# Kernel tuning notes

Measured on AMD Instinct MI355X. Metric: run time of the kernel, lower is better.

## Reference

```python
import jax, jax.numpy as jnp
from jax import lax
import numpy as np

NUM_TAGS = 16
B, S = 512, 4096


def setup_inputs() -> dict:
    key = jax.random.key(0)
    k1, k2, k3, k4, k5 = jax.random.split(key, 5)
    emissions = jax.random.normal(k1, (B, S, NUM_TAGS), dtype=jnp.float32)
    tags = jax.random.randint(k2, (B, S), 0, NUM_TAGS, dtype=jnp.int64)
    mask = jnp.ones((B, S), dtype=bool)
    transitions = jax.random.normal(k3, (NUM_TAGS, NUM_TAGS), dtype=jnp.float32)
    start_transitions = jax.random.normal(k4, (NUM_TAGS,), dtype=jnp.float32)
    end_transitions = jax.random.normal(k5, (NUM_TAGS,), dtype=jnp.float32)
    return {
        "emissions": emissions,
        "tags": tags,
        "mask": mask,
        "transitions": transitions,
        "start_transitions": start_transitions,
        "end_transitions": end_transitions,
    }


def _forward_algorithm(emissions, mask, transitions, start_transitions, end_transitions):
    # emissions: [B,S,T], mask: [B,S] bool
    alphas0 = start_transitions[None, :] + emissions[:, 0]  # [B,T]

    def step(alphas, inp):
        emit_t, mask_t = inp  # [B,T], [B]
        # next_tag_var[b, prev, next] = alphas[b,prev] + transitions[prev,next] + emit[b,next]
        nxt = alphas[:, :, None] + transitions[None, :, :] + emit_t[:, None, :]
        new_alphas = jax.nn.logsumexp(nxt, axis=1)  # [B,T]
        alphas = jnp.where(mask_t[:, None], new_alphas, alphas)
        return alphas, None

    xs = (jnp.swapaxes(emissions, 0, 1)[1:], jnp.swapaxes(mask, 0, 1)[1:])
    alphas, _ = lax.scan(step, alphas0, xs)
    alphas = alphas + end_transitions[None, :]
    return jax.nn.logsumexp(alphas, axis=1)  # [B]


def _score_sentence(emissions, tags, mask, transitions, start_transitions, end_transitions):
    # vectorized version of the per-step torch loop (same math)
    emit_scores = jnp.take_along_axis(emissions, tags[:, :, None], axis=2)[..., 0]  # [B,S]
    trans_scores = transitions[tags[:, :-1], tags[:, 1:]]  # [B,S-1]
    maskf = mask.astype(emissions.dtype)
    scores = start_transitions[tags[:, 0]] + emit_scores[:, 0]
    scores = scores + jnp.sum((trans_scores + emit_scores[:, 1:]) * maskf[:, 1:], axis=1)
    last_valid_idx = jnp.sum(mask.astype(jnp.int32), axis=1) - 1  # [B]
    last_tag = jnp.take_along_axis(tags, last_valid_idx[:, None].astype(tags.dtype), axis=1)[:, 0]
    scores = scores + end_transitions[last_tag]
    return scores  # [B]


def reference(emissions, tags, mask, transitions, start_transitions, end_transitions):
    forward_score = _forward_algorithm(emissions, mask, transitions, start_transitions, end_transitions)
    gold_score = _score_sentence(emissions, tags, mask, transitions, start_transitions, end_transitions)
    return jnp.mean(forward_score - gold_score)  # CRF negative log-likelihood
```

## Files before the change

kernel.cpp:

```cpp
#include <hip/hip_runtime.h>

#define NT 16
#define BB 512
#define SS 4096
#define CL 128
#define NCHAIN 4
#define CLC (CL/NCHAIN)
#define NCH 32
#define NCHUNKS (BB*NCH)
#define NGRP 8
#define NGROUPS (NCHUNKS/NGRP)
#define NSUP (NCH/NGRP)
#define LOG2E 1.44269504088896340736f
#define LN2   0.69314718055994530942f

typedef float v4f __attribute__((ext_vector_type(4)));
typedef float v2f __attribute__((ext_vector_type(2)));
typedef short v4s __attribute__((ext_vector_type(4)));
typedef unsigned v2u __attribute__((ext_vector_type(2)));

#define MFMA16(A,B,C) __builtin_amdgcn_mfma_f32_16x16x16bf16_1k(A,B,C,0,0,0)

static __device__ __forceinline__ unsigned pk2bf(float x, float y) {
    return __builtin_amdgcn_perm(__float_as_uint(y), __float_as_uint(x),
                                 0x07060302u);
}

static __device__ __forceinline__ v4s identity_bfrag(int g, int j) {
    unsigned lo = 0u, hi = 0u;
    if (4 * g + 0 == j) lo |= 0x3F80u;
    if (4 * g + 1 == j) lo |= 0x3F800000u;
    if (4 * g + 2 == j) hi |= 0x3F80u;
    if (4 * g + 3 == j) hi |= 0x3F800000u;
    v2u bp; bp.x = lo; bp.y = hi;
    return __builtin_bit_cast(v4s, bp);
}

__global__ __launch_bounds__(256) void k_chunks(
    const float* __restrict__ em, const int* __restrict__ tags,
    const float* __restrict__ trans, const float* __restrict__ startt,
    const float* __restrict__ endt,
    float* __restrict__ ws_mat, float* __restrict__ ws_gold,
    float* __restrict__ ws_scale)
{
    __shared__ float wbuf[4][CL * NT];
    const int lane  = threadIdx.x & 63;
    const int wv    = threadIdx.x >> 6;
    const int chunk = blockIdx.x * 4 + wv;
    const int b = chunk >> 5;
    const int c = chunk & 31;
    const int j = lane & 15;
    const int g = lane >> 4;
    const int t0 = c * CL + 1;
    const int nst = min(CL, (SS - 1) - c * CL);

    const float* erow = em + (size_t)b * SS * NT;
    float* wf = wbuf[wv];

    {
        const float4* gp4 = (const float4*)(erow + t0 * NT);
        const int maxf = (((SS - t0) * NT) >> 2) - 1;
        #pragma unroll
        for (int kk = 0; kk < (CL * NT / 4) / 64; ++kk) {
            const int f = lane + kk * 64;
            const float4 x = gp4[min(f, maxf)];
            float4 e;
            e.x = __builtin_amdgcn_exp2f(x.x * LOG2E);
            e.y = __builtin_amdgcn_exp2f(x.y * LOG2E);
            e.z = __builtin_amdgcn_exp2f(x.z * LOG2E);
            e.w = __builtin_amdgcn_exp2f(x.w * LOG2E);
            *(float4*)(wf + (f << 2)) = e;
        }
    }

    v2u apc;
    apc.x = pk2bf(
        __builtin_amdgcn_exp2f(trans[(4*g+0)*NT + j] * LOG2E - 5.0f),
        __builtin_amdgcn_exp2f(trans[(4*g+1)*NT + j] * LOG2E - 5.0f));
    apc.y = pk2bf(
        __builtin_amdgcn_exp2f(trans[(4*g+2)*NT + j] * LOG2E - 5.0f),
        __builtin_amdgcn_exp2f(trans[(4*g+3)*NT + j] * LOG2E - 5.0f));
    const v4s afrag = __builtin_bit_cast(v4s, apc);

    v4s bf[NCHAIN];
    v4f ac[NCHAIN];
    #pragma unroll
    for (int q = 0; q < NCHAIN; ++q) {
        bf[q] = identity_bfrag(g, j);
        ac[q] = (v4f){0.f, 0.f, 0.f, 0.f};
    }
    const float* wg = wf + 4 * g;

    #define STEP(q, s) do {                                                \
        v4f t = MFMA16(afrag, bf[q], ((v4f){0.f, 0.f, 0.f, 0.f}));         \
        const float4 w4 = *(const float4*)(wg + (s) * NT);                 \
        t[0] *= w4.x; t[1] *= w4.y; t[2] *= w4.z; t[3] *= w4.w;            \
        ac[q] = t;                                                         \
        v2u p;                                                             \
        p.x = pk2bf(t[0], t[1]);                                           \
        p.y = pk2bf(t[2], t[3]);                                           \
        bf[q] = __builtin_bit_cast(v4s, p);                                \
    } while (0)

    if (nst == CL) {
        #pragma unroll 2
        for (int s = 0; s < CLC; ++s) {
            STEP(0, s);
            STEP(1, CLC + s);
            STEP(2, 2 * CLC + s);
            STEP(3, 3 * CLC + s);
        }
    } else {
        #pragma unroll
        for (int q = 0; q < NCHAIN; ++q) {
            const int lo = q * CLC, hi = min(lo + CLC, nst);
            for (int s = lo; s < hi; ++s) STEP(q, s);
        }
    }
    #undef STEP

    #pragma unroll
    for (int q = 1; q < NCHAIN; ++q)
        #pragma unroll
        for (int r = 0; r < 4; ++r)
            wf[(q - 1) * 256 + (4 * g + r) * NT + j] = ac[q][r];

    v4s run = bf[0];
    v4f accf = ac[0];
    #pragma unroll
    for (int q = 1; q < NCHAIN; ++q) {
        const float4 x = *(const float4*)(wf + (q - 1) * 256 + j * NT + 4 * g);
        v2u ap;
        ap.x = pk2bf(x.x, x.y);
        ap.y = pk2bf(x.z, x.w);
        accf = MFMA16(__builtin_bit_cast(v4s, ap), run,
                      ((v4f){0.f, 0.f, 0.f, 0.f}));
        v2u p;
        p.x = pk2bf(accf[0], accf[1]);
        p.y = pk2bf(accf[2], accf[3]);
        run = __builtin_bit_cast(v4s, p);
    }

    const unsigned u0 = __builtin_amdgcn_readfirstlane(__float_as_uint(accf[0]));
    const int kk = (int)((u0 >> 23) & 0xffu) - 127;
    const float sc = __uint_as_float((unsigned)(127 - kk) << 23);
    float* mp = ws_mat + ((size_t)chunk << 8);
    #pragma unroll
    for (int r = 0; r < 4; ++r)
        mp[(4 * g + r) * NT + j] = accf[r] * sc;
    if (lane == 0) ws_scale[chunk] = (float)kk;

    const int* tg = tags + b * SS;
    float gp = 0.f;
    {
        int t = t0 + lane;
        if (lane < nst) {
            const int tt = tg[t], tp = tg[t - 1];
            gp = trans[tp * NT + tt] + erow[t * NT + tt];
            if (t == SS - 1) gp += endt[tt];
        }
        t = t0 + 64 + lane;
        if (64 + lane < nst) {
            const int tt = tg[t], tp = tg[t - 1];
            gp += trans[tp * NT + tt] + erow[t * NT + tt];
            if (t == SS - 1) gp += endt[tt];
        }
    }
    if (c == 0 && lane == 0) {
        const int z = tg[0];
        gp += startt[z] + erow[z];
    }
    #pragma unroll
    for (int m = 32; m > 0; m >>= 1) gp += __shfl_xor(gp, m, 64);
    if (lane == 0) ws_gold[chunk] = gp;
}

__global__ __launch_bounds__(256) void k_group(
    const float* __restrict__ ws_mat, float* __restrict__ ws2)
{
    const int lane = threadIdx.x & 63;
    const int wid  = blockIdx.x * 4 + (threadIdx.x >> 6);
    const int j = lane & 15;
    const int g = lane >> 4;
    const float* src = ws_mat + ((size_t)wid << 11) + (j << 4) + (g << 2);

    v4s bfrag = identity_bfrag(g, j);
    v4f acc = {0.f, 0.f, 0.f, 0.f};

    #pragma unroll
    for (int m = 0; m < NGRP; ++m) {
        const float4 x = *(const float4*)(src + (m << 8));
        v2u ap;
        ap.x = pk2bf(x.x, x.y);
        ap.y = pk2bf(x.z, x.w);
        acc = MFMA16(__builtin_bit_cast(v4s, ap), bfrag,
                     ((v4f){0.f, 0.f, 0.f, 0.f}));
        v2u p;
        p.x = pk2bf(acc[0], acc[1]);
        p.y = pk2bf(acc[2], acc[3]);
        bfrag = __builtin_bit_cast(v4s, p);
    }

    float* dst = ws2 + ((size_t)wid << 8);
    #pragma unroll
    for (int r = 0; r < 4; ++r)
        dst[(4 * g + r) * NT + j] = acc[r];
}

__global__ __launch_bounds__(256) void k_combine(
    const float* __restrict__ em, const float* __restrict__ startt,
    const float* __restrict__ endt, const float* __restrict__ ws2,
    const float* __restrict__ ws_gold, const float* __restrict__ ws_scale,
    float* __restrict__ ws_fwd)
{
    const int l = threadIdx.x & 63;
    const int j = l & 15;
    const int base = l & 48;
    const int s = (blockIdx.x * 256 + threadIdx.x) >> 4;

    float v = startt[j] + em[(size_t)s * SS * NT + j];
    float m0 = v;
    #pragma unroll
    for (int m = 1; m < 16; m <<= 1) m0 = fmaxf(m0, __shfl_xor(m0, m, 64));
    float lin = exp2f((v - m0) * LOG2E);
    float off = m0 * LOG2E;

    const float* mp = ws2 + ((size_t)s << 10) + (j << 4);
    #pragma unroll
    for (int c = 0; c < NSUP; ++c) {
        const float4* q4 = (const float4*)(mp + (c << 8));
        const float4 q0 = q4[0], q1 = q4[1], q2 = q4[2], q3 = q4[3];
        float accv = 0.f;
        #define TERM(i, comp) accv += __shfl(lin, base | (i), 64) * (comp);
        TERM(0,  q0.x) TERM(1,  q0.y) TERM(2,  q0.z) TERM(3,  q0.w)
        TERM(4,  q1.x) TERM(5,  q1.y) TERM(6,  q1.z) TERM(7,  q1.w)
        TERM(8,  q2.x) TERM(9,  q2.y) TERM(10, q2.z) TERM(11, q2.w)
        TERM(12, q3.x) TERM(13, q3.y) TERM(14, q3.z) TERM(15, q3.w)
        #undef TERM
        float mx = accv;
        #pragma unroll
        for (int m = 1; m < 16; m <<= 1) mx = fmaxf(mx, __shfl_xor(mx, m, 64));
        lin = accv / mx;
        off += log2f(mx);
    }
    float z = lin * exp2f(endt[j] * LOG2E);

    float r = LN2 * (ws_scale[s * NCH + j] + ws_scale[s * NCH + 16 + j])
            - (ws_gold[s * NCH + j] + ws_gold[s * NCH + 16 + j]);

    #pragma unroll
    for (int m = 1; m < 16; m <<= 1) {
        z += __shfl_xor(z, m, 64);
        r += __shfl_xor(r, m, 64);
    }
    if (j == 0)
        ws_fwd[s] = (off + log2f(z) + 5.0f * (float)(SS - 1)) * LN2 + r;
}

__global__ __launch_bounds__(256) void k_final(
    const float* __restrict__ ws_fwd, float* __restrict__ out)
{
    __shared__ float red[256];
    const int tid = threadIdx.x;
    float s = ws_fwd[tid] + ws_fwd[tid + 256];
    red[tid] = s;
    __syncthreads();
    for (int k = 128; k > 0; k >>= 1) {
        if (tid < k) red[tid] += red[tid + k];
        __syncthreads();
    }
    if (tid == 0) out[0] = red[0] * (1.0f / (float)BB);
}

extern "C" void kernel_launch(void* const* d_in, const int* in_sizes, int n_in,
                              void* d_out, int out_size, void* d_ws, size_t ws_size,
                              hipStream_t stream) {
    const float* em     = (const float*)d_in[0];
    const int*   tags   = (const int*)  d_in[1];
    const float* trans  = (const float*)d_in[3];
    const float* startt = (const float*)d_in[4];
    const float* endt   = (const float*)d_in[5];
    float* out = (float*)d_out;

    float* wsf      = (float*)d_ws;
    float* ws_mat   = wsf;
    float* ws2      = ws_mat + (size_t)NCHUNKS * 256;
    float* ws_gold  = ws2 + (size_t)NGROUPS * 256;
    float* ws_scale = ws_gold + NCHUNKS;
    float* ws_fwd   = ws_scale + NCHUNKS;

    k_chunks <<<NCHUNKS / 4, 256, 0, stream>>>(em, tags, trans, startt, endt,
                                               ws_mat, ws_gold, ws_scale);
    k_group  <<<NGROUPS / 4, 256, 0, stream>>>(ws_mat, ws2);
    k_combine<<<BB * NT / 256, 256, 0, stream>>>(em, startt, endt, ws2,
                                                 ws_gold, ws_scale, ws_fwd);
    k_final  <<<1, 256, 0, stream>>>(ws_fwd, out);
}
```

Measured before the change: 225.2 us.

## Fold emission scaling into MFMA A operand and transpose emission buffer

Measured after the change: 226.5 us. No clear change (+0.6%).

```diff
diff --git a/kernel.cpp b/kernel.cpp
--- a/kernel.cpp
+++ b/kernel.cpp
@@ -11,6 +11,7 @@
 #define NGRP 8
 #define NGROUPS (NCHUNKS/NGRP)
 #define NSUP (NCH/NGRP)
+#define WROW 132
 #define LOG2E 1.44269504088896340736f
 #define LN2   0.69314718055994530942f
 
@@ -43,7 +44,7 @@
     float* __restrict__ ws_mat, float* __restrict__ ws_gold,
     float* __restrict__ ws_scale)
 {
-    __shared__ float wbuf[4][CL * NT];
+    __shared__ __align__(16) float wbuf[4][NT * WROW];
     const int lane  = threadIdx.x & 63;
     const int wv    = threadIdx.x >> 6;
     const int chunk = blockIdx.x * 4 + wv;
@@ -64,23 +65,21 @@
         for (int kk = 0; kk < (CL * NT / 4) / 64; ++kk) {
             const int f = lane + kk * 64;
             const float4 x = gp4[min(f, maxf)];
-            float4 e;
-            e.x = __builtin_amdgcn_exp2f(x.x * LOG2E);
-            e.y = __builtin_amdgcn_exp2f(x.y * LOG2E);
-            e.z = __builtin_amdgcn_exp2f(x.z * LOG2E);
-            e.w = __builtin_amdgcn_exp2f(x.w * LOG2E);
-            *(float4*)(wf + (f << 2)) = e;
-        }
-    }
-
-    v2u apc;
-    apc.x = pk2bf(
-        __builtin_amdgcn_exp2f(trans[(4*g+0)*NT + j] * LOG2E - 5.0f),
-        __builtin_amdgcn_exp2f(trans[(4*g+1)*NT + j] * LOG2E - 5.0f));
-    apc.y = pk2bf(
-        __builtin_amdgcn_exp2f(trans[(4*g+2)*NT + j] * LOG2E - 5.0f),
-        __builtin_amdgcn_exp2f(trans[(4*g+3)*NT + j] * LOG2E - 5.0f));
-    const v4s afrag = __builtin_bit_cast(v4s, apc);
+            const int tt = f >> 2;
+            const int jj = (f & 3) << 2;
+            float* dst = wf + jj * WROW + tt;
+            dst[0 * WROW] = __builtin_amdgcn_exp2f(x.x * LOG2E);
+            dst[1 * WROW] = __builtin_amdgcn_exp2f(x.y * LOG2E);
+            dst[2 * WROW] = __builtin_amdgcn_exp2f(x.z * LOG2E);
+            dst[3 * WROW] = __builtin_amdgcn_exp2f(x.w * LOG2E);
+        }
+    }
+
+    v2f e01, e23;
+    e01.x = __builtin_amdgcn_exp2f(trans[(4*g+0)*NT + j] * LOG2E - 5.0f);
+    e01.y = __builtin_amdgcn_exp2f(trans[(4*g+1)*NT + j] * LOG2E - 5.0f);
+    e23.x = __builtin_amdgcn_exp2f(trans[(4*g+2)*NT + j] * LOG2E - 5.0f);
+    e23.y = __builtin_amdgcn_exp2f(trans[(4*g+3)*NT + j] * LOG2E - 5.0f);
 
     v4s bf[NCHAIN];
     v4f ac[NCHAIN];
@@ -89,32 +88,40 @@
         bf[q] = identity_bfrag(g, j);
         ac[q] = (v4f){0.f, 0.f, 0.f, 0.f};
     }
-    const float* wg = wf + 4 * g;
-
-    #define STEP(q, s) do {                                                \
-        v4f t = MFMA16(afrag, bf[q], ((v4f){0.f, 0.f, 0.f, 0.f}));         \
-        const float4 w4 = *(const float4*)(wg + (s) * NT);                 \
-        t[0] *= w4.x; t[1] *= w4.y; t[2] *= w4.z; t[3] *= w4.w;            \
+    const float* wj = wf + j * WROW;
+
+    #define STEP(q, wsc) do {                                              \
+        const v2f p0 = e01 * (wsc);                                        \
+        const v2f p1 = e23 * (wsc);                                        \
+        v2u ap_;                                                           \
+        ap_.x = pk2bf(p0.x, p0.y);                                         \
+        ap_.y = pk2bf(p1.x, p1.y);                                         \
+        v4f t = MFMA16(__builtin_bit_cast(v4s, ap_), bf[q],                \
+                       ((v4f){0.f, 0.f, 0.f, 0.f}));                       \
         ac[q] = t;                                                         \
-        v2u p;                                                             \
-        p.x = pk2bf(t[0], t[1]);                                           \
-        p.y = pk2bf(t[2], t[3]);                                           \
-        bf[q] = __builtin_bit_cast(v4s, p);                                \
+        v2u pp;                                                            \
+        pp.x = pk2bf(t[0], t[1]);                                          \
+        pp.y = pk2bf(t[2], t[3]);                                          \
+        bf[q] = __builtin_bit_cast(v4s, pp);                               \
     } while (0)
 
     if (nst == CL) {
         #pragma unroll 2
-        for (int s = 0; s < CLC; ++s) {
-            STEP(0, s);
-            STEP(1, CLC + s);
-            STEP(2, 2 * CLC + s);
-            STEP(3, 3 * CLC + s);
+        for (int s4 = 0; s4 < CLC; s4 += 4) {
+            const float4 wA = *(const float4*)(wj + 0 * CLC + s4);
+            const float4 wB = *(const float4*)(wj + 1 * CLC + s4);
+            const float4 wC = *(const float4*)(wj + 2 * CLC + s4);
+            const float4 wD = *(const float4*)(wj + 3 * CLC + s4);
+            STEP(0, wA.x); STEP(1, wB.x); STEP(2, wC.x); STEP(3, wD.x);
+            STEP(0, wA.y); STEP(1, wB.y); STEP(2, wC.y); STEP(3, wD.y);
+            STEP(0, wA.z); STEP(1, wB.z); STEP(2, wC.z); STEP(3, wD.z);
+            STEP(0, wA.w); STEP(1, wB.w); STEP(2, wC.w); STEP(3, wD.w);
         }
     } else {
         #pragma unroll
         for (int q = 0; q < NCHAIN; ++q) {
             const int lo = q * CLC, hi = min(lo + CLC, nst);
-            for (int s = lo; s < hi; ++s) STEP(q, s);
+            for (int s = lo; s < hi; ++s) STEP(q, wj[s]);
         }
     }
     #undef STEP
```
